# Kernel tuning notes

Measured on AMD Instinct MI355X. Metric: run time of the kernel, lower is better.

Reference implementation:

```python
import jax, jax.numpy as jnp
import numpy as np

FEW_SHOT_K = 5
NUM_CLASSES = 3
SUPPORT_SIZE = 100


def setup_inputs() -> dict:
    key = jax.random.key(0)
    ks = jax.random.split(key, 12)
    B, S, H = 64, 512, 1024
    scale = 0.02
    return {
        "hidden_states": jax.random.normal(ks[0], (B, S, H), jnp.float32),
        "labels": jax.random.randint(ks[1], (B,), 0, NUM_CLASSES),
        "support_features": jax.random.normal(ks[2], (SUPPORT_SIZE, H), jnp.float32),
        "support_labels": jax.random.randint(ks[3], (SUPPORT_SIZE,), 0, NUM_CLASSES),
        "W_sim": jax.random.normal(ks[4], (128, H), jnp.float32) * scale,
        "b_sim": jnp.zeros((128,), jnp.float32),
        "W_div": jax.random.normal(ks[5], (128, H), jnp.float32) * scale,
        "b_div": jnp.zeros((128,), jnp.float32),
        "W_meta": jax.random.normal(ks[6], (H, H), jnp.float32) * scale,
        "b_meta": jnp.zeros((H,), jnp.float32),
        "W_con": jax.random.normal(ks[7], (256, H), jnp.float32) * scale,
        "b_con": jnp.zeros((256,), jnp.float32),
    }


def reference(hidden_states, labels, support_features, support_labels,
              W_sim, b_sim, W_div, b_div, W_meta, b_meta, W_con, b_con):
    B, S, H = hidden_states.shape
    pooled = hidden_states.mean(axis=1)                       # [B,H] sentence/query features
    similarity_features = pooled @ W_sim.T + b_sim            # [B,128]
    diversity_features = pooled @ W_div.T + b_div             # [B,128]
    meta = jnp.einsum('bsh,oh->bso', hidden_states, W_meta) + b_meta  # [B,S,H]
    meta_contrastive = meta.mean(axis=1) @ W_con.T + b_con    # [B,256]

    # update_support_set: circular buffer write starting at ptr=0, B<100 -> plain slice.
    # Features are .detach()'d in torch before storage.
    supF = support_features.at[:B].set(jax.lax.stop_gradient(pooled))
    supL = support_labels.at[:B].set(labels)

    # topk similarity + softmax weights
    sims = pooled @ supF.T                                    # [B,100]
    top_v, top_i = jax.lax.top_k(sims, FEW_SHOT_K)            # [B,K]
    weights = jax.nn.softmax(top_v, axis=1)                   # [B,K]
    sel_labels = supL[top_i]                                  # [B,K]

    # vectorized replacement of the per-element python scatter loop:
    # pred[b,c] = sum_i weights[b,i] * [sel_labels[b,i] == c], 0<=label<3 guard
    # jax.nn.one_hot yields all-zeros for out-of-range labels, matching the guard.
    onehot = jax.nn.one_hot(sel_labels, NUM_CLASSES, dtype=weights.dtype)  # [B,K,3]
    pred = jnp.einsum('bkc,bk->bc', onehot, weights)          # [B,3]
    few_shot_predictions = jnp.broadcast_to(pred[:, None, :], (B, S, NUM_CLASSES))

    return few_shot_predictions, similarity_features, diversity_features, meta_contrastive
```

## Files before the change

kernel.cpp:

```cpp
#include <hip/hip_runtime.h>

#define BB 64
#define SS 512
#define HH 1024
#define SUP 100
#define KFS 5
#define NCLS 3
#define SEG 16

__global__ void pool_partial(const float* __restrict__ hs, float* __restrict__ part) {
    int blk = blockIdx.x;
    int b   = blk >> 4;
    int seg = blk & (SEG - 1);
    int t   = threadIdx.x;
    const float4* src = (const float4*)(hs + (size_t)b * SS * HH);
    float4 acc = make_float4(0.f, 0.f, 0.f, 0.f);
    int s0 = seg * (SS / SEG);
    for (int s = s0; s < s0 + (SS / SEG); ++s) {
        float4 v = src[s * 256 + t];
        acc.x += v.x; acc.y += v.y; acc.z += v.z; acc.w += v.w;
    }
    ((float4*)part)[(seg * BB + b) * 256 + t] = acc;
}

__global__ void pool_reduce(const float* __restrict__ part, float* __restrict__ pooled) {
    int b = blockIdx.x;
    int t = threadIdx.x;
    float4 acc = make_float4(0.f, 0.f, 0.f, 0.f);
    for (int seg = 0; seg < SEG; ++seg) {
        float4 v = ((const float4*)part)[(seg * BB + b) * 256 + t];
        acc.x += v.x; acc.y += v.y; acc.z += v.z; acc.w += v.w;
    }
    const float inv = 1.0f / 512.0f;
    acc.x *= inv; acc.y *= inv; acc.z *= inv; acc.w *= inv;
    ((float4*)pooled)[b * 256 + t] = acc;
}

__device__ __forceinline__ void linear_tile(const float* __restrict__ A,
                                            const float* __restrict__ W,
                                            const float* __restrict__ bias,
                                            float* __restrict__ out, int N,
                                            int m0, int n0, int t,
                                            float (*As)[68], float (*Bs)[68]) {
    int lr = t >> 4;
    int lc = t & 15;
    int tm = t >> 4, tn = t & 15;
    float acc = 0.f;
    for (int kc = 0; kc < HH; kc += 64) {
        float4 a = *(const float4*)(A + (size_t)(m0 + lr) * HH + kc + lc * 4);
        float4 w = *(const float4*)(W + (size_t)(n0 + lr) * HH + kc + lc * 4);
        *(float4*)&As[lr][lc * 4] = a;
        *(float4*)&Bs[lr][lc * 4] = w;
        __syncthreads();
#pragma unroll
        for (int k = 0; k < 64; ++k)
            acc += As[tm][k] * Bs[tn][k];
        __syncthreads();
    }
    out[(size_t)(m0 + tm) * N + n0 + tn] = acc + bias[n0 + tn];
}

__global__ void linears3(const float* __restrict__ pooled,
                         const float* __restrict__ W_sim, const float* __restrict__ b_sim,
                         const float* __restrict__ W_div, const float* __restrict__ b_div,
                         const float* __restrict__ W_met, const float* __restrict__ b_met,
                         float* __restrict__ out_sim, float* __restrict__ out_div,
                         float* __restrict__ meta_mean) {
    __shared__ __align__(16) float As[16][68];
    __shared__ __align__(16) float Bs[16][68];
    int bx = blockIdx.x;
    const float *W, *bias; float* out; int N, n0;
    if (bx < 8)       { W = W_sim; bias = b_sim; out = out_sim;  N = 128;  n0 = bx * 16; }
    else if (bx < 16) { W = W_div; bias = b_div; out = out_div;  N = 128;  n0 = (bx - 8) * 16; }
    else              { W = W_met; bias = b_met; out = meta_mean; N = 1024; n0 = (bx - 16) * 16; }
    linear_tile(pooled, W, bias, out, N, blockIdx.y * 16, n0, threadIdx.x, As, Bs);
}

__global__ void tail4(const float* __restrict__ meta_mean,
                      const float* __restrict__ W_con, const float* __restrict__ b_con,
                      float* __restrict__ out_con,
                      const float* __restrict__ pooled,
                      const float* __restrict__ supF,
                      const int* __restrict__ labels,
                      const int* __restrict__ supL,
                      float* __restrict__ out_fsp) {
    __shared__ __align__(16) float As[16][68];
    __shared__ __align__(16) float Bs[16][68];
    __shared__ float ps[HH];
    __shared__ float sims[SUP];
    __shared__ float pred[NCLS];
    int blk = blockIdx.x, t = threadIdx.x;

    if (blk >= BB) {
        int id = blk - BB;
        linear_tile(meta_mean, W_con, b_con, out_con, 256,
                    (id >> 4) * 16, (id & 15) * 16, t, As, Bs);
        return;
    }

    int b = blk;
    ((float4*)ps)[t] = ((const float4*)(pooled + (size_t)b * HH))[t];
    __syncthreads();

    int wave = t >> 6, lane = t & 63;
    for (int j = wave; j < SUP; j += 4) {
        const float* row = (j < BB) ? (pooled + (size_t)j * HH)
                                    : (supF + (size_t)j * HH);
        float s = 0.f;
#pragma unroll
        for (int q = 0; q < 16; ++q) {
            int h = lane + q * 64;
            s += ps[h] * row[h];
        }
        for (int off = 32; off; off >>= 1) s += __shfl_down(s, off);
        if (lane == 0) sims[j] = s;
    }
    __syncthreads();

    if (t == 0) {
        float vals[KFS]; int idx[KFS];
        for (int i = 0; i < KFS; ++i) {
            float best = -3.4e38f; int bi = 0;
            for (int j = 0; j < SUP; ++j) {
                bool taken = false;
                for (int p = 0; p < i; ++p) taken = taken || (idx[p] == j);
                if (!taken && sims[j] > best) { best = sims[j]; bi = j; }
            }
            vals[i] = best; idx[i] = bi;
        }
        float mx = vals[0];
        for (int i = 1; i < KFS; ++i) mx = fmaxf(mx, vals[i]);
        float e[KFS], sum = 0.f;
        for (int i = 0; i < KFS; ++i) { e[i] = __expf(vals[i] - mx); sum += e[i]; }
        float p0 = 0.f, p1 = 0.f, p2 = 0.f;
        for (int i = 0; i < KFS; ++i) {
            int j = idx[i];
            int lab = (j < BB) ? labels[j] : supL[j];
            float wv = e[i] / sum;
            if (lab == 0) p0 += wv;
            else if (lab == 1) p1 += wv;
            else if (lab == 2) p2 += wv;
        }
        pred[0] = p0; pred[1] = p1; pred[2] = p2;
    }
    __syncthreads();

    float p[NCLS] = {pred[0], pred[1], pred[2]};
    for (int i = t; i < SS * NCLS; i += 256) {
        int c = i - (i / NCLS) * NCLS;
        out_fsp[(size_t)b * SS * NCLS + i] = p[c];
    }
}

extern "C" void kernel_launch(void* const* d_in, const int* in_sizes, int n_in,
                              void* d_out, int out_size, void* d_ws, size_t ws_size,
                              hipStream_t stream) {
    const float* hs    = (const float*)d_in[0];
    const int*   lab   = (const int*)  d_in[1];
    const float* supF  = (const float*)d_in[2];
    const int*   supL  = (const int*)  d_in[3];
    const float* W_sim = (const float*)d_in[4];
    const float* b_sim = (const float*)d_in[5];
    const float* W_div = (const float*)d_in[6];
    const float* b_div = (const float*)d_in[7];
    const float* W_met = (const float*)d_in[8];
    const float* b_met = (const float*)d_in[9];
    const float* W_con = (const float*)d_in[10];
    const float* b_con = (const float*)d_in[11];

    float* out = (float*)d_out;
    float* out_fsp  = out;
    float* out_sim  = out + 98304;
    float* out_div  = out + 106496;
    float* out_con  = out + 114688;

    float* ws       = (float*)d_ws;
    float* part     = ws;
    float* pooled   = ws + SEG * BB * HH;
    float* meta_mean= pooled + BB * HH;

    pool_partial<<<BB * SEG, 256, 0, stream>>>(hs, part);
    pool_reduce <<<BB,       256, 0, stream>>>(part, pooled);
    linears3<<<dim3(80, 4), 256, 0, stream>>>(pooled, W_sim, b_sim, W_div, b_div,
                                              W_met, b_met, out_sim, out_div, meta_mean);
    tail4<<<128, 256, 0, stream>>>(meta_mean, W_con, b_con, out_con,
                                   pooled, supF, lab, supL, out_fsp);
}
```

Before: 84.31 us.

## Split-K register-tiled GEMMs with combine kernel and finer pooling segments

Replaces the 16x16 one-output-per-thread linear tiles with 64x64 tiles using 4x4 register blocking and split-K over 8 slices, writing partial sums to workspace. A new combine kernel reduces the partials and adds the biases. The W_con GEMM now sums the meta partials on the fly as it loads its A operand. Pooling also uses 32 sequence segments instead of 16 with an unrolled loop. The aim is to cut redundant weight reloads and raise arithmetic intensity. In exchange it adds an extra launch and workspace traffic for the partial sums.

New measurement: 83.14 us. Within noise of the previous version (-1.4%).

```diff
diff --git a/kernel.cpp b/kernel.cpp
--- a/kernel.cpp
+++ b/kernel.cpp
@@ -6,16 +6,21 @@
 #define SUP 100
 #define KFS 5
 #define NCLS 3
-#define SEG 16
+#define SEG 32
+#define KSPLIT 8
+#define KB (HH / KSPLIT)
+#define KC 32
+#define ASLD 68
 
 __global__ void pool_partial(const float* __restrict__ hs, float* __restrict__ part) {
     int blk = blockIdx.x;
-    int b   = blk >> 4;
+    int b   = blk >> 5;
     int seg = blk & (SEG - 1);
     int t   = threadIdx.x;
     const float4* src = (const float4*)(hs + (size_t)b * SS * HH);
     float4 acc = make_float4(0.f, 0.f, 0.f, 0.f);
     int s0 = seg * (SS / SEG);
+#pragma unroll
     for (int s = s0; s < s0 + (SS / SEG); ++s) {
         float4 v = src[s * 256 + t];
         acc.x += v.x; acc.y += v.y; acc.z += v.z; acc.w += v.w;
@@ -36,56 +41,82 @@
     ((float4*)pooled)[b * 256 + t] = acc;
 }
 
-__device__ __forceinline__ void linear_tile(const float* __restrict__ A,
-                                            const float* __restrict__ W,
-                                            const float* __restrict__ bias,
-                                            float* __restrict__ out, int N,
-                                            int m0, int n0, int t,
-                                            float (*As)[68], float (*Bs)[68]) {
-    int lr = t >> 4;
-    int lc = t & 15;
+__device__ __forceinline__ void gemm64_partial(const float* __restrict__ A,
+                                               const float* __restrict__ W,
+                                               float* __restrict__ partOut, int N,
+                                               int n0, int k0, int ks, int t,
+                                               float (*As)[ASLD], float (*Bs)[ASLD]) {
     int tm = t >> 4, tn = t & 15;
-    float acc = 0.f;
-    for (int kc = 0; kc < HH; kc += 64) {
-        float4 a = *(const float4*)(A + (size_t)(m0 + lr) * HH + kc + lc * 4);
-        float4 w = *(const float4*)(W + (size_t)(n0 + lr) * HH + kc + lc * 4);
-        *(float4*)&As[lr][lc * 4] = a;
-        *(float4*)&Bs[lr][lc * 4] = w;
+    int lr = t >> 2, lq = t & 3;
+    float acc[4][4] = {};
+    for (int kc = 0; kc < KB; kc += KC) {
+        int ka = k0 + kc + lq * 4;
+        float4 a0 = *(const float4*)(A + (size_t)lr * HH + ka);
+        float4 a1 = *(const float4*)(A + (size_t)lr * HH + ka + 16);
+        float4 w0 = *(const float4*)(W + (size_t)(n0 + lr) * HH + ka);
+        float4 w1 = *(const float4*)(W + (size_t)(n0 + lr) * HH + ka + 16);
+        As[lq * 4 + 0][lr] = a0.x; As[lq * 4 + 1][lr] = a0.y;
+        As[lq * 4 + 2][lr] = a0.z; As[lq * 4 + 3][lr] = a0.w;
+        As[16 + lq * 4 + 0][lr] = a1.x; As[16 + lq * 4 + 1][lr] = a1.y;
+        As[16 + lq * 4 + 2][lr] = a1.z; As[16 + lq * 4 + 3][lr] = a1.w;
+        Bs[lq * 4 + 0][lr] = w0.x; Bs[lq * 4 + 1][lr] = w0.y;
+        Bs[lq * 4 + 2][lr] = w0.z; Bs[lq * 4 + 3][lr] = w0.w;
+        Bs[16 + lq * 4 + 0][lr] = w1.x; Bs[16 + lq * 4 + 1][lr] = w1.y;
+        Bs[16 + lq * 4 + 2][lr] = w1.z; Bs[16 + lq * 4 + 3][lr] = w1.w;
         __syncthreads();
 #pragma unroll
-        for (int k = 0; k < 64; ++k)
-            acc += As[tm][k] * Bs[tn][k];
+        for (int k = 0; k < KC; ++k) {
+            float4 a4 = *(const float4*)&As[k][tm * 4];
+            float4 b4 = *(const float4*)&Bs[k][tn * 4];
+            acc[0][0] += a4.x * b4.x; acc[0][1] += a4.x * b4.y;
+            acc[0][2] += a4.x * b4.z; acc[0][3] += a4.x * b4.w;
+            acc[1][0] += a4.y * b4.x; acc[1][1] += a4.y * b4.y;
+            acc[1][2] += a4.y * b4.z; acc[1][3] += a4.y * b4.w;
+            acc[2][0] += a4.z * b4.x; acc[2][1] += a4.z * b4.y;
+            acc[2][2] += a4.z * b4.z; acc[2][3] += a4.z * b4.w;
+            acc[3][0] += a4.w * b4.x; acc[3][1] += a4.w * b4.y;
+            acc[3][2] += a4.w * b4.z; acc[3][3] += a4.w * b4.w;
+        }
         __syncthreads();
     }
-    out[(size_t)(m0 + tm) * N + n0 + tn] = acc + bias[n0 + tn];
-}
-
-__global__ void linears3(const float* __restrict__ pooled,
-                         const float* __restrict__ W_sim, const float* __restrict__ b_sim,
-                         const float* __restrict__ W_div, const float* __restrict__ b_div,
-                         const float* __restrict__ W_met, const float* __restrict__ b_met,
-                         float* __restrict__ out_sim, float* __restrict__ out_div,
-                         float* __restrict__ meta_mean) {
-    __shared__ __align__(16) float As[16][68];
-    __shared__ __align__(16) float Bs[16][68];
-    int bx = blockIdx.x;
-    const float *W, *bias; float* out; int N, n0;
-    if (bx < 8)       { W = W_sim; bias = b_sim; out = out_sim;  N = 128;  n0 = bx * 16; }
-    else if (bx < 16) { W = W_div; bias = b_div; out = out_div;  N = 128;  n0 = (bx - 8) * 16; }
-    else              { W = W_met; bias = b_met; out = meta_mean; N = 1024; n0 = (bx - 16) * 16; }
-    linear_tile(pooled, W, bias, out, N, blockIdx.y * 16, n0, threadIdx.x, As, Bs);
-}
-
-__global__ void tail4(const float* __restrict__ meta_mean,
-                      const float* __restrict__ W_con, const float* __restrict__ b_con,
-                      float* __restrict__ out_con,
-                      const float* __restrict__ pooled,
-                      const float* __restrict__ supF,
-                      const int* __restrict__ labels,
-                      const int* __restrict__ supL,
-                      float* __restrict__ out_fsp) {
-    __shared__ __align__(16) float As[16][68];
-    __shared__ __align__(16) float Bs[16][68];
+#pragma unroll
+    for (int i = 0; i < 4; ++i) {
+        float4 o = make_float4(acc[i][0], acc[i][1], acc[i][2], acc[i][3]);
+        *(float4*)(partOut + ((size_t)ks * 64 + tm * 4 + i) * N + n0 + tn * 4) = o;
+    }
+}
+
+__global__ void lin_partial(const float* __restrict__ pooled,
+                            const float* __restrict__ W_sim,
+                            const float* __restrict__ W_div,
+                            const float* __restrict__ W_met,
+                            float* __restrict__ pSim, float* __restrict__ pDiv,
+                            float* __restrict__ pMet) {
+    __shared__ __align__(16) float As[KC][ASLD];
+    __shared__ __align__(16) float Bs[KC][ASLD];
+    int b = blockIdx.x, t = threadIdx.x;
+    if (b < 16) {
+        gemm64_partial(pooled, W_sim, pSim, 128, (b >> 3) * 64, (b & 7) * KB, b & 7, t, As, Bs);
+    } else if (b < 32) {
+        int id = b - 16;
+        gemm64_partial(pooled, W_div, pDiv, 128, (id >> 3) * 64, (id & 7) * KB, id & 7, t, As, Bs);
+    } else {
+        int id = b - 32;
+        gemm64_partial(pooled, W_met, pMet, 1024, (id >> 3) * 64, (id & 7) * KB, id & 7, t, As, Bs);
+    }
+}
+
+__global__ void tail_fewshot_con(const float* __restrict__ pMet,
+                                 const float* __restrict__ b_met,
+                                 const float* __restrict__ W_con,
+                                 float* __restrict__ pCon,
+                                 const float* __restrict__ pooled,
+                                 const float* __restrict__ supF,
+                                 const int* __restrict__ labels,
+                                 const int* __restrict__ supL,
+                                 float* __restrict__ out_fsp) {
+    __shared__ __align__(16) float As[KC][ASLD];
+    __shared__ __align__(16) float Bs[KC][ASLD];
     __shared__ float ps[HH];
     __shared__ float sims[SUP];
     __shared__ float pred[NCLS];
@@ -93,8 +124,52 @@
 
     if (blk >= BB) {
         int id = blk - BB;
-        linear_tile(meta_mean, W_con, b_con, out_con, 256,
-                    (id >> 4) * 16, (id & 15) * 16, t, As, Bs);
+        int n0 = (id >> 3) * 64, ks = id & 7, k0 = ks * KB;
+        int tm = t >> 4, tn = t & 15;
+        int lr = t >> 2, lq = t & 3;
+        float acc[4][4] = {};
+        for (int kc = 0; kc < KB; kc += KC) {
+            int ka = k0 + kc + lq * 4;
+            float4 s0 = *(const float4*)(b_met + ka);
+            float4 s1 = *(const float4*)(b_met + ka + 16);
+#pragma unroll
+            for (int p = 0; p < KSPLIT; ++p) {
+                float4 v0 = *(const float4*)(pMet + ((size_t)p * 64 + lr) * HH + ka);
+                float4 v1 = *(const float4*)(pMet + ((size_t)p * 64 + lr) * HH + ka + 16);
+                s0.x += v0.x; s0.y += v0.y; s0.z += v0.z; s0.w += v0.w;
+                s1.x += v1.x; s1.y += v1.y; s1.z += v1.z; s1.w += v1.w;
+            }
+            float4 w0 = *(const float4*)(W_con + (size_t)(n0 + lr) * HH + ka);
+            float4 w1 = *(const float4*)(W_con + (size_t)(n0 + lr) * HH + ka + 16);
+            As[lq * 4 + 0][lr] = s0.x; As[lq * 4 + 1][lr] = s0.y;
+            As[lq * 4 + 2][lr] = s0.z; As[lq * 4 + 3][lr] = s0.w;
+            As[16 + lq * 4 + 0][lr] = s1.x; As[16 + lq * 4 + 1][lr] = s1.y;
+            As[16 + lq * 4 + 2][lr] = s1.z; As[16 + lq * 4 + 3][lr] = s1.w;
+            Bs[lq * 4 + 0][lr] = w0.x; Bs[lq * 4 + 1][lr] = w0.y;
+            Bs[lq * 4 + 2][lr] = w0.z; Bs[lq * 4 + 3][lr] = w0.w;
+            Bs[16 + lq * 4 + 0][lr] = w1.x; Bs[16 + lq * 4 + 1][lr] = w1.y;
+            Bs[16 + lq * 4 + 2][lr] = w1.z; Bs[16 + lq * 4 + 3][lr] = w1.w;
+            __syncthreads();
+#pragma unroll
+            for (int k = 0; k < KC; ++k) {
+                float4 a4 = *(const float4*)&As[k][tm * 4];
+                float4 b4 = *(const float4*)&Bs[k][tn * 4];
+                acc[0][0] += a4.x * b4.x; acc[0][1] += a4.x * b4.y;
+                acc[0][2] += a4.x * b4.z; acc[0][3] += a4.x * b4.w;
+                acc[1][0] += a4.y * b4.x; acc[1][1] += a4.y * b4.y;
+                acc[1][2] += a4.y * b4.z; acc[1][3] += a4.y * b4.w;
+                acc[2][0] += a4.z * b4.x; acc[2][1] += a4.z * b4.y;
+                acc[2][2] += a4.z * b4.z; acc[2][3] += a4.z * b4.w;
+                acc[3][0] += a4.w * b4.x; acc[3][1] += a4.w * b4.y;
+                acc[3][2] += a4.w * b4.z; acc[3][3] += a4.w * b4.w;
+            }
+            __syncthreads();
+        }
+#pragma unroll
+        for (int i = 0; i < 4; ++i) {
+            float4 o = make_float4(acc[i][0], acc[i][1], acc[i][2], acc[i][3]);
+            *(float4*)(pCon + ((size_t)ks * 64 + tm * 4 + i) * 256 + n0 + tn * 4) = o;
+        }
         return;
     }
 
@@ -149,6 +224,32 @@
     for (int i = t; i < SS * NCLS; i += 256) {
         int c = i - (i / NCLS) * NCLS;
         out_fsp[(size_t)b * SS * NCLS + i] = p[c];
+    }
+}
+
+__global__ void combine(const float* __restrict__ pSim, const float* __restrict__ b_sim,
+                        const float* __restrict__ pDiv, const float* __restrict__ b_div,
+                        const float* __restrict__ pCon, const float* __restrict__ b_con,
+                        float* __restrict__ out_sim, float* __restrict__ out_div,
+                        float* __restrict__ out_con) {
+    int gid = blockIdx.x * 256 + threadIdx.x;
+    if (gid < 8192) {
+        float s = b_sim[gid & 127];
+#pragma unroll
+        for (int p = 0; p < KSPLIT; ++p) s += pSim[p * 8192 + gid];
+        out_sim[gid] = s;
+    } else if (gid < 16384) {
+        int i = gid - 8192;
+        float s = b_div[i & 127];
+#pragma unroll
+        for (int p = 0; p < KSPLIT; ++p) s += pDiv[p * 8192 + i];
+        out_div[i] = s;
+    } else {
+        int i = gid - 16384;
+        float s = b_con[i & 255];
+#pragma unroll
+        for (int p = 0; p < KSPLIT; ++p) s += pCon[p * 16384 + i];
+        out_con[i] = s;
     }
 }
 
@@ -174,15 +275,19 @@
     float* out_div  = out + 106496;
     float* out_con  = out + 114688;
 
-    float* ws       = (float*)d_ws;
-    float* part     = ws;
-    float* pooled   = ws + SEG * BB * HH;
-    float* meta_mean= pooled + BB * HH;
+    float* ws     = (float*)d_ws;
+    float* part   = ws;
+    float* pooled = part + (size_t)SEG * BB * HH;
+    float* pSim   = pooled + BB * HH;
+    float* pDiv   = pSim + KSPLIT * BB * 128;
+    float* pMet   = pDiv + KSPLIT * BB * 128;
+    float* pCon   = pMet + (size_t)KSPLIT * BB * HH;
 
     pool_partial<<<BB * SEG, 256, 0, stream>>>(hs, part);
     pool_reduce <<<BB,       256, 0, stream>>>(part, pooled);
-    linears3<<<dim3(80, 4), 256, 0, stream>>>(pooled, W_sim, b_sim, W_div, b_div,
-                                              W_met, b_met, out_sim, out_div, meta_mean);
-    tail4<<<128, 256, 0, stream>>>(meta_mean, W_con, b_con, out_con,
-                                   pooled, supF, lab, supL, out_fsp);
-}
+    lin_partial <<<160,      256, 0, stream>>>(pooled, W_sim, W_div, W_met, pSim, pDiv, pMet);
+    tail_fewshot_con<<<96,   256, 0, stream>>>(pMet, b_met, W_con, pCon,
+                                               pooled, supF, lab, supL, out_fsp);
+    combine<<<128, 256, 0, stream>>>(pSim, b_sim, pDiv, b_div, pCon, b_con,
+                                     out_sim, out_div, out_con);
+}
```
